# Performance work log

Measured on AMD Instinct MI355X. Metric: run time of the kernel, lower is better.

The kernel has to match this reference:

```python
import jax, jax.numpy as jnp
import numpy as np

NUM_HEADS = 12
THETA = 10000.0


def _rope(x, pos):
    # x: [B, H, S, dk]; interleaved even/odd pair rotation
    dk = x.shape[-1]
    freqs = THETA ** (-jnp.arange(dk // 2, dtype=jnp.float32) * 2.0 / dk)  # [dk/2]
    ang = pos.astype(jnp.float32)[:, None] * freqs                         # [S, dk/2]
    cos, sin = jnp.cos(ang), jnp.sin(ang)
    x1, x2 = x[..., 0::2], x[..., 1::2]
    rot = jnp.stack([x1 * cos - x2 * sin, x1 * sin + x2 * cos], axis=-1)
    return rot.reshape(x.shape)


def setup_inputs() -> dict:
    key = jax.random.key(0)
    ks = jax.random.split(key, 5)
    B, S, D = 4, 2048, 768
    w_scale = 1.0 / np.sqrt(D).astype(np.float32)
    x = jax.random.normal(ks[0], (B, S, D), dtype=jnp.float32)
    Wq = jax.random.normal(ks[1], (D, D), dtype=jnp.float32) * w_scale
    Wk = jax.random.normal(ks[2], (D, D), dtype=jnp.float32) * w_scale
    Wv = jax.random.normal(ks[3], (D, D), dtype=jnp.float32) * w_scale
    Wo = jax.random.normal(ks[4], (D, D), dtype=jnp.float32) * w_scale
    token_positions = jnp.arange(S, dtype=jnp.int32)
    return {"x": x, "Wq": Wq, "Wk": Wk, "Wv": Wv, "Wo": Wo,
            "token_positions": token_positions}


def reference(x, Wq, Wk, Wv, Wo, token_positions):
    B, S, D = x.shape
    H = NUM_HEADS
    dk = D // H
    # bias-free linear layers: y = x @ W^T (torch Linear weight convention)
    q = (x @ Wq.T).reshape(B, S, H, dk).transpose(0, 2, 1, 3)  # [B,H,S,dk]
    k = (x @ Wk.T).reshape(B, S, H, dk).transpose(0, 2, 1, 3)
    v = (x @ Wv.T).reshape(B, S, H, dk).transpose(0, 2, 1, 3)
    q = _rope(q, token_positions)
    k = _rope(k, token_positions)
    scores = jnp.einsum('bhqd,bhkd->bhqk', q, k) / np.float32(np.sqrt(dk))
    causal = jnp.tril(jnp.ones((S, S), dtype=bool))
    scores = jnp.where(causal, scores, -jnp.inf)
    attn = jax.nn.softmax(scores, axis=-1)                      # [B,H,S,S]
    out = jnp.einsum('bhqk,bhkd->bhqd', attn, v)
    out = out.transpose(0, 2, 1, 3).reshape(B, S, D)
    return out @ Wo.T
```

## Files before the change

### kernel.cpp

```cpp
#include <hip/hip_runtime.h>
#include <cstdint>
#include <cstddef>

#define NTOK 8192
#define SLEN 2048
#define DM   768
#define NH   12
#define DKH  64

typedef __attribute__((ext_vector_type(8))) short bf16x8;
typedef __attribute__((ext_vector_type(4))) float f32x4;

__device__ __forceinline__ float b2f(unsigned short u) {
  return __uint_as_float(((unsigned)u) << 16);
}
__device__ __forceinline__ unsigned short f2b(float f) {
  unsigned u = __float_as_uint(f);
  u += 0x7fffu + ((u >> 16) & 1u);
  return (unsigned short)(u >> 16);
}
__device__ __forceinline__ unsigned cvtpk(float lo, float hi) {
  unsigned r;
  asm("v_cvt_pk_bf16_f32 %0, %1, %2" : "=v"(r) : "v"(lo), "v"(hi));
  return r;
}

__device__ __forceinline__ void gld16(const void* g, void* l) {
  __builtin_amdgcn_global_load_lds(
      (const __attribute__((address_space(1))) void*)g,
      (__attribute__((address_space(3))) void*)l, 16, 0, 0);
}

#define BAR_DRAIN() do {                                  \
    asm volatile("s_waitcnt vmcnt(0)" ::: "memory");      \
    __builtin_amdgcn_s_barrier();                         \
    __builtin_amdgcn_sched_barrier(0);                    \
  } while (0)
#define BAR_KEEP4() do {                                  \
    asm volatile("s_waitcnt vmcnt(4)" ::: "memory");      \
    __builtin_amdgcn_s_barrier();                         \
    __builtin_amdgcn_sched_barrier(0);                    \
  } while (0)

__global__ void cast_bf16_kernel(const float* __restrict__ in,
                                 unsigned short* __restrict__ out, int n8) {
  int i = blockIdx.x * blockDim.x + threadIdx.x;
  if (i >= n8) return;
  const float4* p = (const float4*)(in + (size_t)i * 8);
  float4 a = p[0], b = p[1];
  union { unsigned short h[8]; bf16x8 v; } u;
  u.h[0] = f2b(a.x); u.h[1] = f2b(a.y); u.h[2] = f2b(a.z); u.h[3] = f2b(a.w);
  u.h[4] = f2b(b.x); u.h[5] = f2b(b.y); u.h[6] = f2b(b.z); u.h[7] = f2b(b.w);
  *(bf16x8*)(out + (size_t)i * 8) = u.v;
}

__global__ void cast4_bf16_kernel(const float* __restrict__ s0,
                                  const float* __restrict__ s1,
                                  const float* __restrict__ s2,
                                  const float* __restrict__ s3,
                                  unsigned short* __restrict__ out, int n8) {
  int i = blockIdx.x * blockDim.x + threadIdx.x;
  if (i >= n8) return;
  const float* src = (blockIdx.y == 0) ? s0 : (blockIdx.y == 1) ? s1
                    : (blockIdx.y == 2) ? s2 : s3;
  unsigned short* o = out + (size_t)blockIdx.y * DM * DM + (size_t)i * 8;
  const float4* p = (const float4*)(src + (size_t)i * 8);
  float4 a = p[0], b = p[1];
  union { unsigned short h[8]; bf16x8 v; } u;
  u.h[0] = f2b(a.x); u.h[1] = f2b(a.y); u.h[2] = f2b(a.z); u.h[3] = f2b(a.w);
  u.h[4] = f2b(b.x); u.h[5] = f2b(b.y); u.h[6] = f2b(b.z); u.h[7] = f2b(b.w);
  *(bf16x8*)o = u.v;
}

template <typename CT>
__global__ __launch_bounds__(256, 2) void gemm_bt_kernel(
    const unsigned short* __restrict__ A,
    const unsigned short* __restrict__ B0, const unsigned short* __restrict__ B1,
    const unsigned short* __restrict__ B2,
    CT* __restrict__ C0, CT* __restrict__ C1, CT* __restrict__ C2,
    int N, int K, const int* __restrict__ pos, int do_rope) {
  const unsigned short* Bp = (blockIdx.z == 0) ? B0 : (blockIdx.z == 1) ? B1 : B2;
  CT* Cp = (blockIdx.z == 0) ? C0 : (blockIdx.z == 1) ? C1 : C2;
  const int tid = threadIdx.x, wid = tid >> 6, lane = tid & 63;
  const int lrow = lane & 15, g = lane >> 4, lk8 = g * 8;
  const int m0 = blockIdx.y * 128, n0 = blockIdx.x * 128;
  const int wm = (wid >> 1) * 64, wn = (wid & 1) * 64;
  const int sr = lane >> 3, sc = (lane & 7) * 8;
  __shared__ unsigned short At[128 * 64];
  __shared__ unsigned short Bt[128 * 64];
  f32x4 acc[4][4] = {};
  for (int k0 = 0; k0 < K; k0 += 64) {
    __syncthreads();
#pragma unroll
    for (int i = 0; i < 4; ++i) {
      int r = (wid * 4 + i) * 8 + sr;
      int k = sc ^ ((r & 7) << 3);
      gld16(A  + (size_t)(m0 + r) * K + k0 + k, &At[(wid * 4 + i) * 512]);
      gld16(Bp + (size_t)(n0 + r) * K + k0 + k, &Bt[(wid * 4 + i) * 512]);
    }
    __syncthreads();
    bf16x8 af[2][4], bfr[2][4];
#pragma unroll
    for (int ks = 0; ks < 2; ++ks)
#pragma unroll
      for (int mi = 0; mi < 4; ++mi) {
        int ra = wm + mi * 16 + lrow;
        af[ks][mi]  = *(const bf16x8*)&At[ra * 64 + ((ks * 32 + lk8) ^ ((ra & 7) << 3))];
        int rb = wn + mi * 16 + lrow;
        bfr[ks][mi] = *(const bf16x8*)&Bt[rb * 64 + ((ks * 32 + lk8) ^ ((rb & 7) << 3))];
      }
#pragma unroll
    for (int ks = 0; ks < 2; ++ks)
#pragma unroll
      for (int mi = 0; mi < 4; ++mi)
#pragma unroll
        for (int ni = 0; ni < 4; ++ni)
          acc[mi][ni] = __builtin_amdgcn_mfma_f32_16x16x32_bf16(
              bfr[ks][ni], af[ks][mi], acc[mi][ni], 0, 0, 0);
  }

  const bool ropeq = do_rope && (blockIdx.z < 2);
  if (ropeq) {
    float frq[4][2];
#pragma unroll
    for (int ni = 0; ni < 4; ++ni)
#pragma unroll
      for (int rp = 0; rp < 2; ++rp)
        frq[ni][rp] = exp2f(
            (float)(((wn + ni * 16 + g * 4 + rp * 2) & 63) >> 1) *
            -0.4152410118609203f);
#pragma unroll
    for (int mi = 0; mi < 4; ++mi) {
      const int m = m0 + wm + mi * 16 + lrow;
      const float ps = (float)pos[m & (SLEN - 1)];
#pragma unroll
      for (int ni = 0; ni < 4; ++ni)
#pragma unroll
        for (int rp = 0; rp < 2; ++rp) {
          float sn, cs;
          __sincosf(ps * frq[ni][rp], &sn, &cs);
          float x1 = acc[mi][ni][2 * rp], x2 = acc[mi][ni][2 * rp + 1];
          acc[mi][ni][2 * rp]     = fmaf(x1, cs, -x2 * sn);
          acc[mi][ni][2 * rp + 1] = fmaf(x1, sn, x2 * cs);
        }
    }
  }

#pragma unroll
  for (int mi = 0; mi < 4; ++mi) {
    const int m = m0 + wm + mi * 16 + lrow;
#pragma unroll
    for (int ni = 0; ni < 4; ++ni) {
      const int nb = n0 + wn + ni * 16 + g * 4;
      if constexpr (sizeof(CT) == 2) {
        union { unsigned u[2]; ushort4 s; } o;
        o.u[0] = cvtpk(acc[mi][ni][0], acc[mi][ni][1]);
        o.u[1] = cvtpk(acc[mi][ni][2], acc[mi][ni][3]);
        *(ushort4*)&Cp[(size_t)m * N + nb] = o.s;
      } else {
        *(f32x4*)&Cp[(size_t)m * N + nb] = acc[mi][ni];
      }
    }
  }
}

__global__ void transpose_v_kernel(const unsigned short* __restrict__ V,
                                   unsigned short* __restrict__ VT) {
  const int tt = blockIdx.x, bh = blockIdx.y;
  const int b = bh / NH, h = bh - b * NH;
  const unsigned short* src = V + ((size_t)b * SLEN + tt * 64) * DM + h * DKH;
  unsigned short* dst = VT + (size_t)bh * DKH * SLEN + tt * 64;
  __shared__ unsigned short lds[64][72];
  const int tid = threadIdx.x;
  const int r = tid >> 2, cq = tid & 3;
#pragma unroll
  for (int pass = 0; pass < 2; ++pass) {
    int c = cq * 8 + pass * 32;
    *(bf16x8*)&lds[r][c] = *(const bf16x8*)&src[(size_t)r * DM + c];
  }
  __syncthreads();
  const int d = tid >> 2;
#pragma unroll
  for (int pass = 0; pass < 2; ++pass) {
    int s0 = cq * 8 + pass * 32;
    union { unsigned short h[8]; bf16x8 v; } o;
#pragma unroll
    for (int j = 0; j < 8; ++j) {
      int pi = pass * 32 + 16 * (j >> 2) + 4 * cq + (j & 3);
      o.h[j] = lds[pi][d];
    }
    *(bf16x8*)&dst[(size_t)d * SLEN + s0] = o.v;
  }
}

__global__ __launch_bounds__(256, 2) void attn_kernel(
    const unsigned short* __restrict__ Q, const unsigned short* __restrict__ Kg,
    const unsigned short* __restrict__ VT, unsigned short* __restrict__ O) {
  const int bh = blockIdx.x;
  const int qt = 15 - (int)blockIdx.y;
  const int b = bh / NH, h = bh - b * NH;
  const size_t base = ((size_t)b * SLEN) * DM + h * DKH;
  const size_t vbase = (size_t)bh * DKH * SLEN;
  const int tid = threadIdx.x, wid = tid >> 6, lane = tid & 63;
  const int lrow = lane & 15, g = lane >> 4;

  __shared__ unsigned short Kt[3][64 * 64];
  __shared__ unsigned short Vt[3][64 * 64];

  bf16x8 qf[2][2];
#pragma unroll
  for (int mi = 0; mi < 2; ++mi)
#pragma unroll
    for (int ks = 0; ks < 2; ++ks) {
      const int qrow = qt * 128 + wid * 32 + mi * 16 + lrow;
      union { unsigned short h[8]; bf16x8 v; } u;
      u.v = *(const bf16x8*)&Q[base + (size_t)qrow * DM + ks * 32 + g * 8];
#pragma unroll
      for (int j = 0; j < 8; ++j)
        u.h[j] = f2b(b2f(u.h[j]) * 0.18033688011112042f);
      qf[mi][ks] = u.v;
    }

  union { unsigned short h[8]; bf16x8 v; } one_u;
#pragma unroll
  for (int j = 0; j < 8; ++j) one_u.h[j] = 0x3F80;
  const bf16x8 ones = one_u.v;

  f32x4 oacc[2][4] = {};
  f32x4 l_acc[2] = {};
  float m_run[2] = {-1e30f, -1e30f};
  const int qg0 = qt * 128 + wid * 32 + lrow;
  const int nkt = 2 * qt + 2;

  const int srow = wid * 8 + (lane >> 3);
  const int scol = (lane & 7) * 8;

  auto stage = [&](int kt, int buf) {
#pragma unroll
    for (int rnd = 0; rnd < 2; ++rnd) {
      int r = rnd * 32 + srow;
      int c = scol ^ ((r & 7) << 3);
      gld16(Kg + base + (size_t)(kt * 64 + r) * DM + c,
            &Kt[buf][(rnd * 32 + wid * 8) * 64]);
    }
#pragma unroll
    for (int rnd = 0; rnd < 2; ++rnd) {
      int d = rnd * 32 + srow;
      int c = scol ^ ((d & 7) << 3);
      gld16(VT + vbase + (size_t)d * SLEN + kt * 64 + c,
            &Vt[buf][(rnd * 32 + wid * 8) * 64]);
    }
  };

  auto compute = [&](int kt, int buf) {
    const bool active = !(kt == 2 * qt + 1 && wid < 2);
    if (!active) return;
    f32x4 sa[2][4] = {};
    const unsigned short* Ks = Kt[buf];
    __builtin_amdgcn_s_setprio(1);
#pragma unroll
    for (int ks = 0; ks < 2; ++ks)
#pragma unroll
      for (int ni = 0; ni < 4; ++ni) {
        const int krow = ni * 16 + lrow;
        bf16x8 kf = *(const bf16x8*)
            &Ks[krow * 64 + ((ks * 32 + g * 8) ^ ((krow & 7) << 3))];
#pragma unroll
        for (int mi = 0; mi < 2; ++mi)
          sa[mi][ni] = __builtin_amdgcn_mfma_f32_16x16x32_bf16(
              kf, qf[mi][ks], sa[mi][ni], 0, 0, 0);
      }
    __builtin_amdgcn_s_setprio(0);

    const bool need_mask = (kt * 64 + 64 > qt * 128 + wid * 32);
    if (need_mask) {
      const int kb = kt * 64 + g * 4;
#pragma unroll
      for (int mi = 0; mi < 2; ++mi) {
        const int qg = qg0 + mi * 16;
#pragma unroll
        for (int ni = 0; ni < 4; ++ni)
#pragma unroll
          for (int r = 0; r < 4; ++r)
            if (kb + ni * 16 + r > qg) sa[mi][ni][r] = -1e30f;
      }
    }

    float mx[2];
#pragma unroll
    for (int mi = 0; mi < 2; ++mi) {
      f32x4 t01, t23;
#pragma unroll
      for (int r = 0; r < 4; ++r) {
        t01[r] = fmaxf(sa[mi][0][r], sa[mi][1][r]);
        t23[r] = fmaxf(sa[mi][2][r], sa[mi][3][r]);
      }
      float a = fmaxf(fmaxf(t01[0], t23[0]), fmaxf(t01[1], t23[1]));
      float c = fmaxf(fmaxf(t01[2], t23[2]), fmaxf(t01[3], t23[3]));
      mx[mi] = fmaxf(a, c);
    }

    const int viol = (mx[0] > m_run[0] + 8.f) || (mx[1] > m_run[1] + 8.f);
    if (__any(viol)) {
#pragma unroll
      for (int mi = 0; mi < 2; ++mi) {
        float mr = fmaxf(mx[mi], __shfl_xor(mx[mi], 16));
        mr = fmaxf(mr, __shfl_xor(mr, 32));
        float mn = fmaxf(m_run[mi], mr);
        float scl = exp2f(m_run[mi] - mn);
        m_run[mi] = mn;
        l_acc[mi] *= scl;
#pragma unroll
        for (int ni = 0; ni < 4; ++ni) oacc[mi][ni] *= scl;
      }
    }

#pragma unroll
    for (int mi = 0; mi < 2; ++mi)
#pragma unroll
      for (int ni = 0; ni < 4; ++ni)
#pragma unroll
        for (int r = 0; r < 4; ++r)
          sa[mi][ni][r] = exp2f(sa[mi][ni][r] - m_run[mi]);

    bf16x8 pf[2][2];
#pragma unroll
    for (int mi = 0; mi < 2; ++mi)
#pragma unroll
      for (int ks = 0; ks < 2; ++ks) {
        union { unsigned u[4]; bf16x8 v; } uu;
        uu.u[0] = cvtpk(sa[mi][2 * ks][0],     sa[mi][2 * ks][1]);
        uu.u[1] = cvtpk(sa[mi][2 * ks][2],     sa[mi][2 * ks][3]);
        uu.u[2] = cvtpk(sa[mi][2 * ks + 1][0], sa[mi][2 * ks + 1][1]);
        uu.u[3] = cvtpk(sa[mi][2 * ks + 1][2], sa[mi][2 * ks + 1][3]);
        pf[mi][ks] = uu.v;
      }

    const unsigned short* Vs = Vt[buf];
    __builtin_amdgcn_s_setprio(1);
#pragma unroll
    for (int ks = 0; ks < 2; ++ks) {
#pragma unroll
      for (int ni = 0; ni < 4; ++ni) {
        const int d = ni * 16 + lrow;
        bf16x8 vf = *(const bf16x8*)
            &Vs[d * 64 + ((ks * 32 + g * 8) ^ ((d & 7) << 3))];
#pragma unroll
        for (int mi = 0; mi < 2; ++mi)
          oacc[mi][ni] = __builtin_amdgcn_mfma_f32_16x16x32_bf16(
              vf, pf[mi][ks], oacc[mi][ni], 0, 0, 0);
      }
#pragma unroll
      for (int mi = 0; mi < 2; ++mi)
        l_acc[mi] = __builtin_amdgcn_mfma_f32_16x16x32_bf16(
            ones, pf[mi][ks], l_acc[mi], 0, 0, 0);
    }
    __builtin_amdgcn_s_setprio(0);
  };

  stage(0, 0);
  for (int kt = 0; kt < nkt; ++kt) {
    if (kt + 1 < nkt) {
      stage(kt + 1, (kt + 1) % 3);
      BAR_KEEP4();
    } else {
      BAR_DRAIN();
    }
    compute(kt, kt % 3);
  }

#pragma unroll
  for (int mi = 0; mi < 2; ++mi) {
    const float inv = 1.f / l_acc[mi][0];
    const int qrow = qt * 128 + wid * 32 + mi * 16 + lrow;
#pragma unroll
    for (int ni = 0; ni < 4; ++ni) {
      union { unsigned u[2]; ushort4 s; } o;
      o.u[0] = cvtpk(oacc[mi][ni][0] * inv, oacc[mi][ni][1] * inv);
      o.u[1] = cvtpk(oacc[mi][ni][2] * inv, oacc[mi][ni][3] * inv);
      *(ushort4*)&O[base + (size_t)qrow * DM + ni * 16 + g * 4] = o.s;
    }
  }
}

extern "C" void kernel_launch(void* const* d_in, const int* in_sizes, int n_in,
                              void* d_out, int out_size, void* d_ws, size_t ws_size,
                              hipStream_t stream) {
  const float* x  = (const float*)d_in[0];
  const float* Wq = (const float*)d_in[1];
  const float* Wk = (const float*)d_in[2];
  const float* Wv = (const float*)d_in[3];
  const float* Wo = (const float*)d_in[4];
  const int* pos  = (const int*)d_in[5];
  float* out = (float*)d_out;

  char* ws = (char*)d_ws;
  size_t off = 0;
  auto carve = [&](size_t bytes) -> void* {
    void* p = ws + off;
    off += (bytes + 255) & ~(size_t)255;
    return p;
  };
  unsigned short* xb  = (unsigned short*)carve((size_t)NTOK * DM * 2);
  unsigned short* wqb = (unsigned short*)carve((size_t)DM * DM * 2);
  unsigned short* wkb = (unsigned short*)carve((size_t)DM * DM * 2);
  unsigned short* wvb = (unsigned short*)carve((size_t)DM * DM * 2);
  unsigned short* wob = (unsigned short*)carve((size_t)DM * DM * 2);
  unsigned short* Qb  = (unsigned short*)carve((size_t)NTOK * DM * 2);
  unsigned short* Kb  = (unsigned short*)carve((size_t)NTOK * DM * 2);
  unsigned short* Vb  = (unsigned short*)carve((size_t)NTOK * DM * 2);
  unsigned short* Ab  = (unsigned short*)carve((size_t)NTOK * DM * 2);
  unsigned short* VTb = (unsigned short*)carve((size_t)4 * NH * DKH * SLEN * 2);

  const int n8x = NTOK * DM / 8;
  const int n8w = DM * DM / 8;
  cast_bf16_kernel<<<dim3((n8x + 255) / 256), dim3(256), 0, stream>>>(x, xb, n8x);
  cast4_bf16_kernel<<<dim3((n8w + 255) / 256, 4), dim3(256), 0, stream>>>(
      Wq, Wk, Wv, Wo, wqb, n8w);

  gemm_bt_kernel<unsigned short><<<dim3(6, 64, 3), dim3(256), 0, stream>>>(
      xb, wqb, wkb, wvb, Qb, Kb, Vb, DM, DM, pos, 1);

  transpose_v_kernel<<<dim3(SLEN / 64, 4 * NH), dim3(256), 0, stream>>>(Vb, VTb);

  attn_kernel<<<dim3(48, 16), dim3(256), 0, stream>>>(Qb, Kb, VTb, Ab);

  gemm_bt_kernel<float><<<dim3(6, 64, 1), dim3(256), 0, stream>>>(
      Ab, wob, wob, wob, out, out, out, DM, DM, pos, 0);
}
```

Baseline: 140.2 us.

## Fuse V transpose into QKV GEMM epilogue, merge casts, halve GEMM M-tile

```diff
diff --git a/kernel.cpp b/kernel.cpp
--- a/kernel.cpp
+++ b/kernel.cpp
@@ -42,85 +42,115 @@
     __builtin_amdgcn_sched_barrier(0);                    \
   } while (0)
 
-__global__ void cast_bf16_kernel(const float* __restrict__ in,
-                                 unsigned short* __restrict__ out, int n8) {
-  int i = blockIdx.x * blockDim.x + threadIdx.x;
-  if (i >= n8) return;
-  const float4* p = (const float4*)(in + (size_t)i * 8);
+__global__ void cast_all_kernel(const float* __restrict__ x,
+                                const float* __restrict__ w0,
+                                const float* __restrict__ w1,
+                                const float* __restrict__ w2,
+                                const float* __restrict__ w3,
+                                unsigned short* __restrict__ xb,
+                                unsigned short* __restrict__ wb) {
+  const int bid = blockIdx.x, tid = threadIdx.x;
+  const float* src;
+  unsigned short* dst;
+  size_t i;
+  if (bid < 3072) {
+    src = x; dst = xb; i = (size_t)bid * 256 + tid;
+  } else {
+    const int wbid = bid - 3072;
+    const int w = wbid / 288;
+    src = (w == 0) ? w0 : (w == 1) ? w1 : (w == 2) ? w2 : w3;
+    dst = wb + (size_t)w * DM * DM;
+    i = (size_t)(wbid - w * 288) * 256 + tid;
+  }
+  const float4* p = (const float4*)(src + i * 8);
   float4 a = p[0], b = p[1];
   union { unsigned short h[8]; bf16x8 v; } u;
   u.h[0] = f2b(a.x); u.h[1] = f2b(a.y); u.h[2] = f2b(a.z); u.h[3] = f2b(a.w);
   u.h[4] = f2b(b.x); u.h[5] = f2b(b.y); u.h[6] = f2b(b.z); u.h[7] = f2b(b.w);
-  *(bf16x8*)(out + (size_t)i * 8) = u.v;
-}
-
-__global__ void cast4_bf16_kernel(const float* __restrict__ s0,
-                                  const float* __restrict__ s1,
-                                  const float* __restrict__ s2,
-                                  const float* __restrict__ s3,
-                                  unsigned short* __restrict__ out, int n8) {
-  int i = blockIdx.x * blockDim.x + threadIdx.x;
-  if (i >= n8) return;
-  const float* src = (blockIdx.y == 0) ? s0 : (blockIdx.y == 1) ? s1
-                    : (blockIdx.y == 2) ? s2 : s3;
-  unsigned short* o = out + (size_t)blockIdx.y * DM * DM + (size_t)i * 8;
-  const float4* p = (const float4*)(src + (size_t)i * 8);
-  float4 a = p[0], b = p[1];
-  union { unsigned short h[8]; bf16x8 v; } u;
-  u.h[0] = f2b(a.x); u.h[1] = f2b(a.y); u.h[2] = f2b(a.z); u.h[3] = f2b(a.w);
-  u.h[4] = f2b(b.x); u.h[5] = f2b(b.y); u.h[6] = f2b(b.z); u.h[7] = f2b(b.w);
-  *(bf16x8*)o = u.v;
+  *(bf16x8*)(dst + i * 8) = u.v;
 }
 
 template <typename CT>
-__global__ __launch_bounds__(256, 2) void gemm_bt_kernel(
+__global__ __launch_bounds__(256, 2) void gemm64_kernel(
     const unsigned short* __restrict__ A,
     const unsigned short* __restrict__ B0, const unsigned short* __restrict__ B1,
     const unsigned short* __restrict__ B2,
     CT* __restrict__ C0, CT* __restrict__ C1, CT* __restrict__ C2,
-    int N, int K, const int* __restrict__ pos, int do_rope) {
+    unsigned short* __restrict__ VTout,
+    int N, int K, const int* __restrict__ pos, int qkv_mode) {
   const unsigned short* Bp = (blockIdx.z == 0) ? B0 : (blockIdx.z == 1) ? B1 : B2;
   CT* Cp = (blockIdx.z == 0) ? C0 : (blockIdx.z == 1) ? C1 : C2;
   const int tid = threadIdx.x, wid = tid >> 6, lane = tid & 63;
   const int lrow = lane & 15, g = lane >> 4, lk8 = g * 8;
-  const int m0 = blockIdx.y * 128, n0 = blockIdx.x * 128;
-  const int wm = (wid >> 1) * 64, wn = (wid & 1) * 64;
-  const int sr = lane >> 3, sc = (lane & 7) * 8;
-  __shared__ unsigned short At[128 * 64];
+  const int m0 = blockIdx.y * 64, n0 = blockIdx.x * 128;
+  const int wm = (wid >> 1) * 32, wn = (wid & 1) * 64;
+  const int sr = wid * 8 + (lane >> 3), sc = (lane & 7) * 8;
+  __shared__ unsigned short At[64 * 64];
   __shared__ unsigned short Bt[128 * 64];
-  f32x4 acc[4][4] = {};
+  f32x4 acc[2][4] = {};
+
   for (int k0 = 0; k0 < K; k0 += 64) {
     __syncthreads();
 #pragma unroll
-    for (int i = 0; i < 4; ++i) {
-      int r = (wid * 4 + i) * 8 + sr;
-      int k = sc ^ ((r & 7) << 3);
-      gld16(A  + (size_t)(m0 + r) * K + k0 + k, &At[(wid * 4 + i) * 512]);
-      gld16(Bp + (size_t)(n0 + r) * K + k0 + k, &Bt[(wid * 4 + i) * 512]);
+    for (int rnd = 0; rnd < 2; ++rnd) {
+      int r = rnd * 32 + sr;
+      int c = sc ^ ((r & 7) << 3);
+      gld16(A + (size_t)(m0 + r) * K + k0 + c, &At[(rnd * 32 + wid * 8) * 64]);
+    }
+#pragma unroll
+    for (int rnd = 0; rnd < 4; ++rnd) {
+      int r = rnd * 32 + sr;
+      int c = sc ^ ((r & 7) << 3);
+      gld16(Bp + (size_t)(n0 + r) * K + k0 + c, &Bt[(rnd * 32 + wid * 8) * 64]);
     }
     __syncthreads();
-    bf16x8 af[2][4], bfr[2][4];
+    bf16x8 af[2][2], bfr[2][4];
+#pragma unroll
+    for (int ks = 0; ks < 2; ++ks) {
+#pragma unroll
+      for (int mi = 0; mi < 2; ++mi) {
+        int ra = wm + mi * 16 + lrow;
+        af[ks][mi] = *(const bf16x8*)&At[ra * 64 + ((ks * 32 + lk8) ^ ((ra & 7) << 3))];
+      }
+#pragma unroll
+      for (int ni = 0; ni < 4; ++ni) {
+        int rb = wn + ni * 16 + lrow;
+        bfr[ks][ni] = *(const bf16x8*)&Bt[rb * 64 + ((ks * 32 + lk8) ^ ((rb & 7) << 3))];
+      }
+    }
 #pragma unroll
     for (int ks = 0; ks < 2; ++ks)
 #pragma unroll
-      for (int mi = 0; mi < 4; ++mi) {
-        int ra = wm + mi * 16 + lrow;
-        af[ks][mi]  = *(const bf16x8*)&At[ra * 64 + ((ks * 32 + lk8) ^ ((ra & 7) << 3))];
-        int rb = wn + mi * 16 + lrow;
-        bfr[ks][mi] = *(const bf16x8*)&Bt[rb * 64 + ((ks * 32 + lk8) ^ ((rb & 7) << 3))];
-      }
-#pragma unroll
-    for (int ks = 0; ks < 2; ++ks)
-#pragma unroll
-      for (int mi = 0; mi < 4; ++mi)
+      for (int mi = 0; mi < 2; ++mi)
 #pragma unroll
         for (int ni = 0; ni < 4; ++ni)
           acc[mi][ni] = __builtin_amdgcn_mfma_f32_16x16x32_bf16(
               bfr[ks][ni], af[ks][mi], acc[mi][ni], 0, 0, 0);
   }
 
-  const bool ropeq = do_rope && (blockIdx.z < 2);
-  if (ropeq) {
+  if (qkv_mode && blockIdx.z == 2) {
+#pragma unroll
+    for (int mi = 0; mi < 2; ++mi) {
+      const int m = m0 + wm + mi * 16 + lrow;
+      const int bb = m >> 11, st = m & (SLEN - 1);
+      const int scol = (st & ~63) | (st & 35) |
+                       (((st >> 4) & 1) << 2) | (((st >> 2) & 1) << 3) |
+                       (((st >> 3) & 1) << 4);
+#pragma unroll
+      for (int ni = 0; ni < 4; ++ni) {
+        const int nb = n0 + wn + ni * 16 + g * 4;
+        const int hh = nb >> 6, dd = nb & 63;
+        unsigned short* dst =
+            VTout + ((size_t)(bb * NH + hh) * DKH + dd) * SLEN + scol;
+#pragma unroll
+        for (int r = 0; r < 4; ++r)
+          dst[(size_t)r * SLEN] = f2b(acc[mi][ni][r]);
+      }
+    }
+    return;
+  }
+
+  if (qkv_mode) {
     float frq[4][2];
 #pragma unroll
     for (int ni = 0; ni < 4; ++ni)
@@ -130,7 +160,7 @@
             (float)(((wn + ni * 16 + g * 4 + rp * 2) & 63) >> 1) *
             -0.4152410118609203f);
 #pragma unroll
-    for (int mi = 0; mi < 4; ++mi) {
+    for (int mi = 0; mi < 2; ++mi) {
       const int m = m0 + wm + mi * 16 + lrow;
       const float ps = (float)pos[m & (SLEN - 1)];
 #pragma unroll
@@ -147,7 +177,7 @@
   }
 
 #pragma unroll
-  for (int mi = 0; mi < 4; ++mi) {
+  for (int mi = 0; mi < 2; ++mi) {
     const int m = m0 + wm + mi * 16 + lrow;
 #pragma unroll
     for (int ni = 0; ni < 4; ++ni) {
@@ -161,35 +191,6 @@
         *(f32x4*)&Cp[(size_t)m * N + nb] = acc[mi][ni];
       }
     }
-  }
-}
-
-__global__ void transpose_v_kernel(const unsigned short* __restrict__ V,
-                                   unsigned short* __restrict__ VT) {
-  const int tt = blockIdx.x, bh = blockIdx.y;
-  const int b = bh / NH, h = bh - b * NH;
-  const unsigned short* src = V + ((size_t)b * SLEN + tt * 64) * DM + h * DKH;
-  unsigned short* dst = VT + (size_t)bh * DKH * SLEN + tt * 64;
-  __shared__ unsigned short lds[64][72];
-  const int tid = threadIdx.x;
-  const int r = tid >> 2, cq = tid & 3;
-#pragma unroll
-  for (int pass = 0; pass < 2; ++pass) {
-    int c = cq * 8 + pass * 32;
-    *(bf16x8*)&lds[r][c] = *(const bf16x8*)&src[(size_t)r * DM + c];
-  }
-  __syncthreads();
-  const int d = tid >> 2;
-#pragma unroll
-  for (int pass = 0; pass < 2; ++pass) {
-    int s0 = cq * 8 + pass * 32;
-    union { unsigned short h[8]; bf16x8 v; } o;
-#pragma unroll
-    for (int j = 0; j < 8; ++j) {
-      int pi = pass * 32 + 16 * (j >> 2) + 4 * cq + (j & 3);
-      o.h[j] = lds[pi][d];
-    }
-    *(bf16x8*)&dst[(size_t)d * SLEN + s0] = o.v;
   }
 }
 
@@ -408,23 +409,17 @@
   unsigned short* wob = (unsigned short*)carve((size_t)DM * DM * 2);
   unsigned short* Qb  = (unsigned short*)carve((size_t)NTOK * DM * 2);
   unsigned short* Kb  = (unsigned short*)carve((size_t)NTOK * DM * 2);
-  unsigned short* Vb  = (unsigned short*)carve((size_t)NTOK * DM * 2);
   unsigned short* Ab  = (unsigned short*)carve((size_t)NTOK * DM * 2);
   unsigned short* VTb = (unsigned short*)carve((size_t)4 * NH * DKH * SLEN * 2);
 
-  const int n8x = NTOK * DM / 8;
-  const int n8w = DM * DM / 8;
-  cast_bf16_kernel<<<dim3((n8x + 255) / 256), dim3(256), 0, stream>>>(x, xb, n8x);
-  cast4_bf16_kernel<<<dim3((n8w + 255) / 256, 4), dim3(256), 0, stream>>>(
-      Wq, Wk, Wv, Wo, wqb, n8w);
-
-  gemm_bt_kernel<unsigned short><<<dim3(6, 64, 3), dim3(256), 0, stream>>>(
-      xb, wqb, wkb, wvb, Qb, Kb, Vb, DM, DM, pos, 1);
-
-  transpose_v_kernel<<<dim3(SLEN / 64, 4 * NH), dim3(256), 0, stream>>>(Vb, VTb);
+  cast_all_kernel<<<dim3(3072 + 4 * 288), dim3(256), 0, stream>>>(
+      x, Wq, Wk, Wv, Wo, xb, wqb);
+
+  gemm64_kernel<unsigned short><<<dim3(6, 128, 3), dim3(256), 0, stream>>>(
+      xb, wqb, wkb, wvb, Qb, Kb, Qb, VTb, DM, DM, pos, 1);
 
   attn_kernel<<<dim3(48, 16), dim3(256), 0, stream>>>(Qb, Kb, VTb, Ab);
 
-  gemm_bt_kernel<float><<<dim3(6, 64, 1), dim3(256), 0, stream>>>(
-      Ab, wob, wob, wob, out, out, out, DM, DM, pos, 0);
-}
+  gemm64_kernel<float><<<dim3(6, 128, 1), dim3(256), 0, stream>>>(
+      Ab, wob, wob, wob, out, out, out, nullptr, DM, DM, pos, 0);
+}
```

Result: faster. 134.6 us (-4.0%).
